# Performance work log

Hardware: AMD Instinct MI355X
Metric: run time of the kernel (lower is better)

## Reference

```python
import jax, jax.numpy as jnp
import numpy as np
import math

LMAX_IN = 3
LMAX_OUT = 2 * LMAX_IN
K_IN = (LMAX_IN + 1) ** 2      # 16
K_OUT = (LMAX_OUT + 1) ** 2    # 49
RES_BETA = 8
RES_ALPHA = 16
N = 1024
MUL = 128
C = 128
PARITY_CONFIGS = [(1, 1), (1, -1), (-1, 1)]


def _legendre(lmax, x):
    # Associated Legendre P_l^m(x) for m >= 0 (Condon-Shortley phase), numpy float64.
    P = np.zeros((lmax + 1, lmax + 1, x.shape[0]))
    s = np.sqrt(np.clip(1.0 - x * x, 0.0, 1.0))
    P[0, 0] = 1.0
    for m in range(1, lmax + 1):
        P[m, m] = -(2 * m - 1) * s * P[m - 1, m - 1]
    for m in range(lmax):
        P[m + 1, m] = (2 * m + 1) * x * P[m, m]
    for m in range(lmax + 1):
        for l in range(m + 2, lmax + 1):
            P[l, m] = ((2 * l - 1) * x * P[l - 1, m] - (l - 1 + m) * P[l - 2, m]) / (l - m)
    return P


def _real_sh(lmax, cosb, alpha):
    # Orthonormal real spherical harmonics on the (beta, alpha) grid -> [(lmax+1)^2, B*A].
    P = _legendre(lmax, cosb)
    B, A = cosb.shape[0], alpha.shape[0]
    Y = np.zeros(((lmax + 1) ** 2, B, A))
    for l in range(lmax + 1):
        for m in range(-l, l + 1):
            am = abs(m)
            norm = math.sqrt((2 * l + 1) / (4 * math.pi) * math.factorial(l - am) / math.factorial(l + am))
            if m > 0:
                az = math.sqrt(2.0) * np.cos(m * alpha)
            elif m == 0:
                az = np.ones(A)
            else:
                az = math.sqrt(2.0) * np.sin(am * alpha)
            Y[l * l + l + m] = norm * P[l, am][:, None] * az[None, :]
    return Y.reshape((lmax + 1) ** 2, B * A)


def _grids():
    # Gauss-Legendre quadrature in cos(beta), uniform azimuth -> exact band-limited transforms.
    cosb, wb = np.polynomial.legendre.leggauss(RES_BETA)
    alpha = np.linspace(0.0, 2.0 * np.pi, RES_ALPHA, endpoint=False)
    qw = (wb[:, None] * np.full((1, RES_ALPHA), 2.0 * np.pi / RES_ALPHA)).reshape(-1)
    Y_in = _real_sh(LMAX_IN, cosb, alpha)
    Y_out_w = _real_sh(LMAX_OUT, cosb, alpha) * qw[None, :]
    return Y_in.astype(np.float32), Y_out_w.astype(np.float32)


def _l_of_k(lmax):
    return np.array([l for l in range(lmax + 1) for _ in range(2 * l + 1)])


_YIN_NP, _YOW_NP = _grids()
_LK_IN = _l_of_k(LMAX_IN)
_LK_OUT = _l_of_k(LMAX_OUT)


def _project_in(x, W, p_val):
    # e3nn.flax.Linear to s2_irreps(lmax, p_val, p_arg=-1)*C : per-l pick the matching
    # parity block of the input and channel-mix it (1/sqrt(fan_in) path norm).
    pi_l = np.array([(1 - p_val * (-1) ** l) // 2 for l in range(LMAX_IN + 1)])
    pi_k = pi_l[_LK_IN]                      # [K_IN] parity slot per SH component
    x_sel = x[:, :, pi_k, np.arange(K_IN)]    # [N, MUL, K_IN]
    Wk = W[_LK_IN]                            # [K_IN, MUL, C]
    return jnp.einsum('nuk,kuc->nck', x_sel, Wk) * (1.0 / math.sqrt(MUL))


def setup_inputs() -> dict:
    key = jax.random.key(0)
    k1, k2, k3, k4, k5 = jax.random.split(key, 5)
    return {
        'input1': jax.random.normal(k1, (N, MUL, 2, K_IN), dtype=jnp.float32),
        'input2': jax.random.normal(k2, (N, MUL, 2, K_IN), dtype=jnp.float32),
        'W_in1': jax.random.normal(k3, (3, LMAX_IN + 1, MUL, C), dtype=jnp.float32),
        'W_in2': jax.random.normal(k4, (3, LMAX_IN + 1, MUL, C), dtype=jnp.float32),
        'W_out': jax.random.normal(k5, (3, LMAX_OUT + 1, C, C), dtype=jnp.float32),
    }


def reference(input1, input2, W_in1, W_in2, W_out):
    Yin = jnp.asarray(_YIN_NP)    # [K_IN, G] synthesis basis
    Yow = jnp.asarray(_YOW_NP)    # [K_OUT, G] analysis basis (quadrature-weighted)
    outs = []
    for i, (p1, p2) in enumerate(PARITY_CONFIGS):
        c1 = _project_in(input1, W_in1[i], p1)           # [N, C, K_IN]
        c2 = _project_in(input2, W_in2[i], p2)           # [N, C, K_IN]
        g1 = jnp.einsum('nck,kg->ncg', c1, Yin)          # SH synthesis on S2 grid
        g2 = jnp.einsum('nck,kg->ncg', c2, Yin)
        z = jnp.einsum('ncg,kg->nck', g1 * g2, Yow)      # pointwise mult + analysis, lmax_out = 2*lmax
        Wo = W_out[i][_LK_OUT]                            # [K_OUT, C, C]
        o = jnp.einsum('nck,kcd->ndk', z, Wo) * (1.0 / math.sqrt(C))
        outs.append(o.reshape(N, C * K_OUT))
    return jnp.concatenate(outs, axis=1)                 # [N, 3*C*K_OUT]
```

## Files before the change

### kernel.cpp

```cpp
#include <hip/hip_runtime.h>
#include <hip/hip_bf16.h>
#include <math.h>


#define PI_D 3.14159265358979323846

using short8 = __attribute__((ext_vector_type(8))) short;
using f32x4  = __attribute__((ext_vector_type(4))) float;

__device__ __host__ constexpr int lof_in(int k)  { return k>=9?3 : k>=4?2 : k>=1?1 : 0; }
__device__ __host__ constexpr int lof_out(int k) { return k>=36?6 : k>=25?5 : k>=16?4 : k>=9?3 : k>=4?2 : k>=1?1 : 0; }

__device__ __forceinline__ unsigned short f2h(float f) {
  _Float16 h = (_Float16)f;
  return __builtin_bit_cast(unsigned short, h);
}

__global__ void tables_kernel(unsigned short* __restrict__ YinH,
                              unsigned short* __restrict__ YowH)
{
  const int g = threadIdx.x;
  if (g >= 128) return;
  const int b = g >> 4;
  const int a = g & 15;

  const double xb_[8] = {
    -0.9602898564975362, -0.7966664774136267, -0.5255324099163290, -0.1834346424956498,
     0.1834346424956498,  0.5255324099163290,  0.7966664774136267,  0.9602898564975362};
  const double wb_[8] = {
     0.10122853629037626, 0.22238103445337447, 0.31370664587788729, 0.36268378337836198,
     0.36268378337836198, 0.31370664587788729, 0.22238103445337447, 0.10122853629037626};

  const double x = xb_[b];
  const double s = sqrt(fmax(0.0, 1.0 - x * x));
  const double alpha = (2.0 * PI_D / 16.0) * (double)a;

  double P[7][7];
  for (int l = 0; l < 7; ++l)
    for (int m = 0; m < 7; ++m) P[l][m] = 0.0;
  P[0][0] = 1.0;
  for (int m = 1; m <= 6; ++m) P[m][m] = -(double)(2 * m - 1) * s * P[m - 1][m - 1];
  for (int m = 0; m <= 5; ++m) P[m + 1][m] = (double)(2 * m + 1) * x * P[m][m];
  for (int m = 0; m <= 6; ++m)
    for (int l = m + 2; l <= 6; ++l)
      P[l][m] = ((double)(2 * l - 1) * x * P[l - 1][m] - (double)(l - 1 + m) * P[l - 2][m]) / (double)(l - m);

  const double qw = wb_[b] * (2.0 * PI_D / 16.0);

  for (int l = 0; l <= 6; ++l) {
    for (int m = -l; m <= l; ++m) {
      const int am = m < 0 ? -m : m;
      double fr = 1.0;
      for (int j = l - am + 1; j <= l + am; ++j) fr /= (double)j;
      const double norm = sqrt((double)(2 * l + 1) / (4.0 * PI_D) * fr);
      double az;
      if (m > 0)       az = sqrt(2.0) * cos((double)m * alpha);
      else if (m == 0) az = 1.0;
      else             az = sqrt(2.0) * sin((double)am * alpha);
      const double Y = norm * P[l][am] * az;
      const int k = l * l + l + m;
      if (l <= 3) YinH[g * 16 + k] = f2h((float)Y);
      YowH[k * 128 + g] = f2h((float)(Y * qw));
    }
  }
  for (int k = 49; k < 64; ++k) YowH[k * 128 + g] = 0;
}

__global__ void prep_wot(const float* __restrict__ Wo, unsigned short* __restrict__ WoTH)
{
  const int e = blockIdx.x * 256 + threadIdx.x;
  const int c = e & 127;
  const int d = (e >> 7) & 127;
  const int r = e >> 14;
  WoTH[((size_t)r * 128 + d) * 128 + c] = f2h(Wo[((size_t)r * 128 + c) * 128 + d]);
}

template <int IP>
__device__ __forceinline__ void stage1_body(
    int nb, int tid, float* lds,
    const float* __restrict__ x1, const float* __restrict__ x2,
    const float* __restrict__ W1, const float* __restrict__ W2,
    unsigned short* __restrict__ c1H, unsigned short* __restrict__ c2H)
{
  const int c  = tid & 127;
  const int nn = tid >> 7;
  const int n  = nb * 2 + nn;

  float c1a[16], c2a[16];
#pragma unroll
  for (int k = 0; k < 16; ++k) { c1a[k] = 0.f; c2a[k] = 0.f; }

  const float* w1b = W1 + IP * 65536 + c;
  const float* w2b = W2 + IP * 65536 + c;

  for (int uc = 0; uc < 4; ++uc) {
    __syncthreads();
#pragma unroll
    for (int i = 0; i < 8; ++i) {
      const int e   = tid + 256 * i;
      const int inp = e >> 10;
      const int r   = e & 1023;
      const int nns = r >> 9;
      const int u   = (r >> 4) & 31;
      const int k   = r & 15;
      const int l   = lof_in(k);
      const int flip = (inp == 0) ? ((IP == 2) ? 1 : 0) : ((IP == 1) ? 1 : 0);
      const int ch  = (l & 1) ^ flip;
      const float* src = (inp == 0) ? x1 : x2;
      lds[e] = src[(size_t)(nb * 2 + nns) * 4096 + uc * 1024 + u * 32 + ch * 16 + k];
    }
    __syncthreads();
    for (int uu = 0; uu < 32; ++uu) {
      const int u = uc * 32 + uu;
      float w1v[4], w2v[4];
#pragma unroll
      for (int l = 0; l < 4; ++l) {
        w1v[l] = w1b[(l * 128 + u) * 128];
        w2v[l] = w2b[(l * 128 + u) * 128];
      }
      const float4* xs1 = (const float4*)&lds[nn * 512 + uu * 16];
      const float4* xs2 = (const float4*)&lds[1024 + nn * 512 + uu * 16];
      const float4 A0 = xs1[0], A1 = xs1[1], A2 = xs1[2], A3 = xs1[3];
      const float4 B0 = xs2[0], B1 = xs2[1], B2 = xs2[2], B3 = xs2[3];
      c1a[0]  = fmaf(A0.x, w1v[0], c1a[0]);
      c1a[1]  = fmaf(A0.y, w1v[1], c1a[1]);
      c1a[2]  = fmaf(A0.z, w1v[1], c1a[2]);
      c1a[3]  = fmaf(A0.w, w1v[1], c1a[3]);
      c1a[4]  = fmaf(A1.x, w1v[2], c1a[4]);
      c1a[5]  = fmaf(A1.y, w1v[2], c1a[5]);
      c1a[6]  = fmaf(A1.z, w1v[2], c1a[6]);
      c1a[7]  = fmaf(A1.w, w1v[2], c1a[7]);
      c1a[8]  = fmaf(A2.x, w1v[2], c1a[8]);
      c1a[9]  = fmaf(A2.y, w1v[3], c1a[9]);
      c1a[10] = fmaf(A2.z, w1v[3], c1a[10]);
      c1a[11] = fmaf(A2.w, w1v[3], c1a[11]);
      c1a[12] = fmaf(A3.x, w1v[3], c1a[12]);
      c1a[13] = fmaf(A3.y, w1v[3], c1a[13]);
      c1a[14] = fmaf(A3.z, w1v[3], c1a[14]);
      c1a[15] = fmaf(A3.w, w1v[3], c1a[15]);

      c2a[0]  = fmaf(B0.x, w2v[0], c2a[0]);
      c2a[1]  = fmaf(B0.y, w2v[1], c2a[1]);
      c2a[2]  = fmaf(B0.z, w2v[1], c2a[2]);
      c2a[3]  = fmaf(B0.w, w2v[1], c2a[3]);
      c2a[4]  = fmaf(B1.x, w2v[2], c2a[4]);
      c2a[5]  = fmaf(B1.y, w2v[2], c2a[5]);
      c2a[6]  = fmaf(B1.z, w2v[2], c2a[6]);
      c2a[7]  = fmaf(B1.w, w2v[2], c2a[7]);
      c2a[8]  = fmaf(B2.x, w2v[2], c2a[8]);
      c2a[9]  = fmaf(B2.y, w2v[3], c2a[9]);
      c2a[10] = fmaf(B2.z, w2v[3], c2a[10]);
      c2a[11] = fmaf(B2.w, w2v[3], c2a[11]);
      c2a[12] = fmaf(B3.x, w2v[3], c2a[12]);
      c2a[13] = fmaf(B3.y, w2v[3], c2a[13]);
      c2a[14] = fmaf(B3.z, w2v[3], c2a[14]);
      c2a[15] = fmaf(B3.w, w2v[3], c2a[15]);
    }
  }

  const float ism = 0.08838834764831845f;
  unsigned int pk1[8], pk2[8];
#pragma unroll
  for (int q = 0; q < 8; ++q) {
    pk1[q] = (unsigned)f2h(c1a[2 * q] * ism) | ((unsigned)f2h(c1a[2 * q + 1] * ism) << 16);
    pk2[q] = (unsigned)f2h(c2a[2 * q] * ism) | ((unsigned)f2h(c2a[2 * q + 1] * ism) << 16);
  }
  const size_t ob = (((size_t)IP * 1024 + n) * 128 + c) * 16;
  uint4* o1 = (uint4*)(c1H + ob);
  uint4* o2 = (uint4*)(c2H + ob);
  o1[0] = make_uint4(pk1[0], pk1[1], pk1[2], pk1[3]);
  o1[1] = make_uint4(pk1[4], pk1[5], pk1[6], pk1[7]);
  o2[0] = make_uint4(pk2[0], pk2[1], pk2[2], pk2[3]);
  o2[1] = make_uint4(pk2[4], pk2[5], pk2[6], pk2[7]);
}

__global__ __launch_bounds__(256, 4) void stage1_kernel(
    const float* __restrict__ x1, const float* __restrict__ x2,
    const float* __restrict__ W1, const float* __restrict__ W2,
    unsigned short* __restrict__ c1H, unsigned short* __restrict__ c2H)
{
  __shared__ float lds[2048];
  const int bid = blockIdx.x;
  const int ip = bid >> 9;
  const int nb = bid & 511;
  const int tid = threadIdx.x;
  if (ip == 0)      stage1_body<0>(nb, tid, lds, x1, x2, W1, W2, c1H, c2H);
  else if (ip == 1) stage1_body<1>(nb, tid, lds, x1, x2, W1, W2, c1H, c2H);
  else              stage1_body<2>(nb, tid, lds, x1, x2, W1, W2, c1H, c2H);
}

__global__ __launch_bounds__(256, 3) void fused23_kernel(
    const unsigned short* __restrict__ c1H, const unsigned short* __restrict__ c2H,
    const unsigned short* __restrict__ YinH, const unsigned short* __restrict__ YowH,
    unsigned short* __restrict__ zH)
{
  __shared__ char Pl[32768];
  const int bid = blockIdx.x;
  const int ip  = bid >> 10;
  const int n   = bid & 1023;
  const int tid = threadIdx.x;
  const int w    = tid >> 6;
  const int lane = tid & 63;
  const int lr   = lane & 15;
  const int lg   = lane >> 4;

  const short8 Z8 = {0, 0, 0, 0, 0, 0, 0, 0};

  short8 a1[2], a2[2];
  const size_t cbase = ((size_t)ip * 1024 + n) * 128 * 16;
#pragma unroll
  for (int mti = 0; mti < 2; ++mti) {
    const int c = (2 * w + mti) * 16 + lr;
    a1[mti] = Z8; a2[mti] = Z8;
    if (lg < 2) {
      a1[mti] = *(const short8*)(c1H + cbase + (size_t)c * 16 + lg * 8);
      a2[mti] = *(const short8*)(c2H + cbase + (size_t)c * 16 + lg * 8);
    }
  }

#pragma unroll
  for (int h = 0; h < 2; ++h) {
    short8 yb[4];
#pragma unroll
    for (int gq = 0; gq < 4; ++gq) {
      const int g = (h * 4 + gq) * 16 + lr;
      yb[gq] = Z8;
      if (lg < 2) yb[gq] = *(const short8*)(YinH + (size_t)g * 16 + lg * 8);
    }
    f32x4 G1[2][4], G2[2][4];
#pragma unroll
    for (int mti = 0; mti < 2; ++mti)
#pragma unroll
      for (int gq = 0; gq < 4; ++gq) {
        G1[mti][gq] = (f32x4){0.f, 0.f, 0.f, 0.f};
        G2[mti][gq] = (f32x4){0.f, 0.f, 0.f, 0.f};
        G1[mti][gq] = __builtin_amdgcn_mfma_f32_16x16x32_f16(a1[mti], yb[gq], G1[mti][gq], 0, 0, 0);
        G2[mti][gq] = __builtin_amdgcn_mfma_f32_16x16x32_f16(a2[mti], yb[gq], G2[mti][gq], 0, 0, 0);
      }
#pragma unroll
    for (int mti = 0; mti < 2; ++mti)
#pragma unroll
      for (int gq = 0; gq < 4; ++gq) {
        const int g = (h * 4 + gq) * 16 + lr;
#pragma unroll
        for (int j = 0; j < 4; ++j) {
          const int m = (2 * w + mti) * 16 + lg * 4 + j;
          const float p = G1[mti][gq][j] * G2[mti][gq][j];
          *(unsigned short*)(Pl + m * 256 + ((g * 2) ^ ((m & 7) << 4))) = f2h(p);
        }
      }
  }
  __syncthreads();

  short8 yw[4][4];
#pragma unroll
  for (int kt = 0; kt < 4; ++kt)
#pragma unroll
    for (int ks = 0; ks < 4; ++ks)
      yw[kt][ks] = *(const short8*)(YowH + (size_t)(kt * 16 + lr) * 128 + ks * 32 + lg * 8);

  f32x4 Zc[2][4];
#pragma unroll
  for (int mti = 0; mti < 2; ++mti)
#pragma unroll
    for (int kt = 0; kt < 4; ++kt) Zc[mti][kt] = (f32x4){0.f, 0.f, 0.f, 0.f};

#pragma unroll
  for (int ks = 0; ks < 4; ++ks) {
    short8 ap[2];
#pragma unroll
    for (int mti = 0; mti < 2; ++mti) {
      const int m = (2 * w + mti) * 16 + lr;
      ap[mti] = *(const short8*)(Pl + m * 256 + ((ks * 64 + lg * 16) ^ ((m & 7) << 4)));
    }
#pragma unroll
    for (int mti = 0; mti < 2; ++mti)
#pragma unroll
      for (int kt = 0; kt < 4; ++kt)
        Zc[mti][kt] = __builtin_amdgcn_mfma_f32_16x16x32_f16(ap[mti], yw[kt][ks], Zc[mti][kt], 0, 0, 0);
  }

#pragma unroll
  for (int mti = 0; mti < 2; ++mti)
#pragma unroll
    for (int kt = 0; kt < 4; ++kt) {
      const int kout = kt * 16 + lr;
      if (kout < 49) {
        const int c0 = (2 * w + mti) * 16 + lg * 4;
        uint2 v;
        v.x = (unsigned)f2h(Zc[mti][kt][0]) | ((unsigned)f2h(Zc[mti][kt][1]) << 16);
        v.y = (unsigned)f2h(Zc[mti][kt][2]) | ((unsigned)f2h(Zc[mti][kt][3]) << 16);
        *(uint2*)(zH + (((size_t)ip * 49 + kout) * 1024 + n) * 128 + c0) = v;
      }
    }
}

__global__ __launch_bounds__(256, 3) void stage4_mfma(
    const unsigned short* __restrict__ zH, const unsigned short* __restrict__ WoTH,
    float* __restrict__ out)
{
  const int bid = blockIdx.x;
  const int ip  = bid / 392;
  const int r   = bid - ip * 392;
  const int w49 = r >> 3;
  const int nblk = r & 7;
  const int l   = lof_out(w49);
  const int tid = threadIdx.x;
  const int wv   = tid >> 6;
  const int lane = tid & 63;
  const int lr   = lane & 15;
  const int lg   = lane >> 4;

  const unsigned short* Ab = zH + (((size_t)ip * 49 + w49) * 1024 + nblk * 128) * 128;
  const unsigned short* Bb = WoTH + (size_t)(ip * 7 + l) * 128 * 128;

  f32x4 acc[2][8];
#pragma unroll
  for (int mti = 0; mti < 2; ++mti)
#pragma unroll
    for (int dt = 0; dt < 8; ++dt) acc[mti][dt] = (f32x4){0.f, 0.f, 0.f, 0.f};

#pragma unroll
  for (int ks = 0; ks < 4; ++ks) {
    short8 b[8], a[2];
#pragma unroll
    for (int dt = 0; dt < 8; ++dt)
      b[dt] = *(const short8*)(Bb + (size_t)(dt * 16 + lr) * 128 + ks * 32 + lg * 8);
#pragma unroll
    for (int mti = 0; mti < 2; ++mti)
      a[mti] = *(const short8*)(Ab + (size_t)((2 * wv + mti) * 16 + lr) * 128 + ks * 32 + lg * 8);
#pragma unroll
    for (int mti = 0; mti < 2; ++mti)
#pragma unroll
      for (int dt = 0; dt < 8; ++dt)
        acc[mti][dt] = __builtin_amdgcn_mfma_f32_16x16x32_f16(a[mti], b[dt], acc[mti][dt], 0, 0, 0);
  }

  const float isc = 0.08838834764831845f;
#pragma unroll
  for (int mti = 0; mti < 2; ++mti)
#pragma unroll
    for (int dt = 0; dt < 8; ++dt) {
      const int d = dt * 16 + lr;
#pragma unroll
      for (int j = 0; j < 4; ++j) {
        const int n = nblk * 128 + (2 * wv + mti) * 16 + lg * 4 + j;
        out[(size_t)n * 18816 + ip * 6272 + d * 49 + w49] = acc[mti][dt][j] * isc;
      }
    }
}

extern "C" void kernel_launch(void* const* d_in, const int* in_sizes, int n_in,
                              void* d_out, int out_size, void* d_ws, size_t ws_size,
                              hipStream_t stream)
{
  const float* x1 = (const float*)d_in[0];
  const float* x2 = (const float*)d_in[1];
  const float* W1 = (const float*)d_in[2];
  const float* W2 = (const float*)d_in[3];
  const float* Wo = (const float*)d_in[4];
  float* out = (float*)d_out;

  char* ws = (char*)d_ws;
  unsigned short* YinH = (unsigned short*)(ws);
  unsigned short* YowH = (unsigned short*)(ws + 16384);
  unsigned short* WoTH = (unsigned short*)(ws + 49152);
  unsigned short* c1H  = (unsigned short*)(ws + (1u << 20));
  unsigned short* c2H  = (unsigned short*)(ws + (1u << 24));
  unsigned short* zH   = (unsigned short*)(ws + (1u << 25));

  tables_kernel<<<1, 128, 0, stream>>>(YinH, YowH);
  prep_wot<<<1344, 256, 0, stream>>>(Wo, WoTH);
  stage1_kernel<<<1536, 256, 0, stream>>>(x1, x2, W1, W2, c1H, c2H);
  fused23_kernel<<<3072, 256, 0, stream>>>(c1H, c2H, YinH, YowH, zH);
  stage4_mfma<<<1176, 256, 0, stream>>>(zH, WoTH, out);
}
```

Baseline: 416.4 us.

## Move input projection to MFMA, parallelize SH tables, restructure output GEMM tiling

Replaces the scalar FMA input projection with fp16 MFMA GEMMs. This needs new kernels that pre-transpose the weights and the inputs into fp16 layouts grouped by k. The table kernel now spreads each (grid point, k) pair across threads instead of one thread looping serially. The output projection kernel is retiled so each block loops over all 49 k values for one d-tile, reusing B fragments per l. Risks: inputs are now quantized to fp16, the new k-major scatter stores to c1H and out are strided, and the extra launches add overhead.

```diff
diff --git a/kernel.cpp b/kernel.cpp
--- a/kernel.cpp
+++ b/kernel.cpp
@@ -16,11 +16,13 @@
   return __builtin_bit_cast(unsigned short, h);
 }
 
-__global__ void tables_kernel(unsigned short* __restrict__ YinH,
-                              unsigned short* __restrict__ YowH)
-{
-  const int g = threadIdx.x;
-  if (g >= 128) return;
+__global__ void tables2(unsigned short* __restrict__ YinH,
+                        unsigned short* __restrict__ YowH)
+{
+  const int g = blockIdx.x;
+  const int t = threadIdx.x;
+  if (t >= 64 || g >= 128) return;
+
   const int b = g >> 4;
   const int a = g & 15;
 
@@ -31,39 +33,40 @@
      0.10122853629037626, 0.22238103445337447, 0.31370664587788729, 0.36268378337836198,
      0.36268378337836198, 0.31370664587788729, 0.22238103445337447, 0.10122853629037626};
 
+  if (t >= 49) {
+    YowH[t * 128 + g] = 0;
+    return;
+  }
+
+  const int l  = lof_out(t);
+  const int m  = t - l * l - l;
+  const int am = m < 0 ? -m : m;
+
   const double x = xb_[b];
   const double s = sqrt(fmax(0.0, 1.0 - x * x));
   const double alpha = (2.0 * PI_D / 16.0) * (double)a;
 
-  double P[7][7];
-  for (int l = 0; l < 7; ++l)
-    for (int m = 0; m < 7; ++m) P[l][m] = 0.0;
-  P[0][0] = 1.0;
-  for (int m = 1; m <= 6; ++m) P[m][m] = -(double)(2 * m - 1) * s * P[m - 1][m - 1];
-  for (int m = 0; m <= 5; ++m) P[m + 1][m] = (double)(2 * m + 1) * x * P[m][m];
-  for (int m = 0; m <= 6; ++m)
-    for (int l = m + 2; l <= 6; ++l)
-      P[l][m] = ((double)(2 * l - 1) * x * P[l - 1][m] - (double)(l - 1 + m) * P[l - 2][m]) / (double)(l - m);
-
+  double pmm = 1.0;
+  for (int j = 1; j <= am; ++j) pmm = -(double)(2 * j - 1) * s * pmm;
+  double p = pmm, pm1 = 0.0;
+  for (int ll = am; ll < l; ++ll) {
+    double pn = ((double)(2 * ll + 1) * x * p - (double)(ll + am) * pm1) / (double)(ll + 1 - am);
+    pm1 = p; p = pn;
+  }
+
+  double fr = 1.0;
+  for (int j = l - am + 1; j <= l + am; ++j) fr /= (double)j;
+  const double norm = sqrt((double)(2 * l + 1) / (4.0 * PI_D) * fr);
+  double az;
+  if (m > 0)       az = sqrt(2.0) * cos((double)m * alpha);
+  else if (m == 0) az = 1.0;
+  else             az = sqrt(2.0) * sin((double)am * alpha);
+
+  const double Y  = norm * p * az;
   const double qw = wb_[b] * (2.0 * PI_D / 16.0);
 
-  for (int l = 0; l <= 6; ++l) {
-    for (int m = -l; m <= l; ++m) {
-      const int am = m < 0 ? -m : m;
-      double fr = 1.0;
-      for (int j = l - am + 1; j <= l + am; ++j) fr /= (double)j;
-      const double norm = sqrt((double)(2 * l + 1) / (4.0 * PI_D) * fr);
-      double az;
-      if (m > 0)       az = sqrt(2.0) * cos((double)m * alpha);
-      else if (m == 0) az = 1.0;
-      else             az = sqrt(2.0) * sin((double)am * alpha);
-      const double Y = norm * P[l][am] * az;
-      const int k = l * l + l + m;
-      if (l <= 3) YinH[g * 16 + k] = f2h((float)Y);
-      YowH[k * 128 + g] = f2h((float)(Y * qw));
-    }
-  }
-  for (int k = 49; k < 64; ++k) YowH[k * 128 + g] = 0;
+  if (t < 16) YinH[g * 16 + t] = f2h((float)Y);
+  YowH[t * 128 + g] = f2h((float)(Y * qw));
 }
 
 __global__ void prep_wot(const float* __restrict__ Wo, unsigned short* __restrict__ WoTH)
@@ -75,118 +78,111 @@
   WoTH[((size_t)r * 128 + d) * 128 + c] = f2h(Wo[((size_t)r * 128 + c) * 128 + d]);
 }
 
-template <int IP>
-__device__ __forceinline__ void stage1_body(
-    int nb, int tid, float* lds,
+__global__ void prep_win(const float* __restrict__ W1, const float* __restrict__ W2,
+                         unsigned short* __restrict__ WtIn)
+{
+  const int e = blockIdx.x * 256 + threadIdx.x;
+  const int u = e & 127;
+  const int c = (e >> 7) & 127;
+  const int r = e >> 14;
+  const int in = r / 12;
+  const int rr = r - in * 12;
+  const float* W = (in == 0) ? W1 : W2;
+  WtIn[e] = f2h(W[((size_t)rr * 128 + u) * 128 + c]);
+}
+
+__global__ __launch_bounds__(256) void transpose_x(
     const float* __restrict__ x1, const float* __restrict__ x2,
-    const float* __restrict__ W1, const float* __restrict__ W2,
-    unsigned short* __restrict__ c1H, unsigned short* __restrict__ c2H)
-{
-  const int c  = tid & 127;
-  const int nn = tid >> 7;
-  const int n  = nb * 2 + nn;
-
-  float c1a[16], c2a[16];
-#pragma unroll
-  for (int k = 0; k < 16; ++k) { c1a[k] = 0.f; c2a[k] = 0.f; }
-
-  const float* w1b = W1 + IP * 65536 + c;
-  const float* w2b = W2 + IP * 65536 + c;
-
-  for (int uc = 0; uc < 4; ++uc) {
-    __syncthreads();
-#pragma unroll
-    for (int i = 0; i < 8; ++i) {
-      const int e   = tid + 256 * i;
-      const int inp = e >> 10;
-      const int r   = e & 1023;
-      const int nns = r >> 9;
-      const int u   = (r >> 4) & 31;
-      const int k   = r & 15;
-      const int l   = lof_in(k);
-      const int flip = (inp == 0) ? ((IP == 2) ? 1 : 0) : ((IP == 1) ? 1 : 0);
-      const int ch  = (l & 1) ^ flip;
-      const float* src = (inp == 0) ? x1 : x2;
-      lds[e] = src[(size_t)(nb * 2 + nns) * 4096 + uc * 1024 + u * 32 + ch * 16 + k];
-    }
-    __syncthreads();
-    for (int uu = 0; uu < 32; ++uu) {
-      const int u = uc * 32 + uu;
-      float w1v[4], w2v[4];
-#pragma unroll
-      for (int l = 0; l < 4; ++l) {
-        w1v[l] = w1b[(l * 128 + u) * 128];
-        w2v[l] = w2b[(l * 128 + u) * 128];
-      }
-      const float4* xs1 = (const float4*)&lds[nn * 512 + uu * 16];
-      const float4* xs2 = (const float4*)&lds[1024 + nn * 512 + uu * 16];
-      const float4 A0 = xs1[0], A1 = xs1[1], A2 = xs1[2], A3 = xs1[3];
-      const float4 B0 = xs2[0], B1 = xs2[1], B2 = xs2[2], B3 = xs2[3];
-      c1a[0]  = fmaf(A0.x, w1v[0], c1a[0]);
-      c1a[1]  = fmaf(A0.y, w1v[1], c1a[1]);
-      c1a[2]  = fmaf(A0.z, w1v[1], c1a[2]);
-      c1a[3]  = fmaf(A0.w, w1v[1], c1a[3]);
-      c1a[4]  = fmaf(A1.x, w1v[2], c1a[4]);
-      c1a[5]  = fmaf(A1.y, w1v[2], c1a[5]);
-      c1a[6]  = fmaf(A1.z, w1v[2], c1a[6]);
-      c1a[7]  = fmaf(A1.w, w1v[2], c1a[7]);
-      c1a[8]  = fmaf(A2.x, w1v[2], c1a[8]);
-      c1a[9]  = fmaf(A2.y, w1v[3], c1a[9]);
-      c1a[10] = fmaf(A2.z, w1v[3], c1a[10]);
-      c1a[11] = fmaf(A2.w, w1v[3], c1a[11]);
-      c1a[12] = fmaf(A3.x, w1v[3], c1a[12]);
-      c1a[13] = fmaf(A3.y, w1v[3], c1a[13]);
-      c1a[14] = fmaf(A3.z, w1v[3], c1a[14]);
-      c1a[15] = fmaf(A3.w, w1v[3], c1a[15]);
-
-      c2a[0]  = fmaf(B0.x, w2v[0], c2a[0]);
-      c2a[1]  = fmaf(B0.y, w2v[1], c2a[1]);
-      c2a[2]  = fmaf(B0.z, w2v[1], c2a[2]);
-      c2a[3]  = fmaf(B0.w, w2v[1], c2a[3]);
-      c2a[4]  = fmaf(B1.x, w2v[2], c2a[4]);
-      c2a[5]  = fmaf(B1.y, w2v[2], c2a[5]);
-      c2a[6]  = fmaf(B1.z, w2v[2], c2a[6]);
-      c2a[7]  = fmaf(B1.w, w2v[2], c2a[7]);
-      c2a[8]  = fmaf(B2.x, w2v[2], c2a[8]);
-      c2a[9]  = fmaf(B2.y, w2v[3], c2a[9]);
-      c2a[10] = fmaf(B2.z, w2v[3], c2a[10]);
-      c2a[11] = fmaf(B2.w, w2v[3], c2a[11]);
-      c2a[12] = fmaf(B3.x, w2v[3], c2a[12]);
-      c2a[13] = fmaf(B3.y, w2v[3], c2a[13]);
-      c2a[14] = fmaf(B3.z, w2v[3], c2a[14]);
-      c2a[15] = fmaf(B3.w, w2v[3], c2a[15]);
-    }
-  }
-
-  const float ism = 0.08838834764831845f;
-  unsigned int pk1[8], pk2[8];
-#pragma unroll
-  for (int q = 0; q < 8; ++q) {
-    pk1[q] = (unsigned)f2h(c1a[2 * q] * ism) | ((unsigned)f2h(c1a[2 * q + 1] * ism) << 16);
-    pk2[q] = (unsigned)f2h(c2a[2 * q] * ism) | ((unsigned)f2h(c2a[2 * q + 1] * ism) << 16);
-  }
-  const size_t ob = (((size_t)IP * 1024 + n) * 128 + c) * 16;
-  uint4* o1 = (uint4*)(c1H + ob);
-  uint4* o2 = (uint4*)(c2H + ob);
-  o1[0] = make_uint4(pk1[0], pk1[1], pk1[2], pk1[3]);
-  o1[1] = make_uint4(pk1[4], pk1[5], pk1[6], pk1[7]);
-  o2[0] = make_uint4(pk2[0], pk2[1], pk2[2], pk2[3]);
-  o2[1] = make_uint4(pk2[4], pk2[5], pk2[6], pk2[7]);
-}
-
-__global__ __launch_bounds__(256, 4) void stage1_kernel(
-    const float* __restrict__ x1, const float* __restrict__ x2,
-    const float* __restrict__ W1, const float* __restrict__ W2,
-    unsigned short* __restrict__ c1H, unsigned short* __restrict__ c2H)
-{
-  __shared__ float lds[2048];
+    unsigned short* __restrict__ xT)
+{
   const int bid = blockIdx.x;
-  const int ip = bid >> 9;
+  const int in = bid >> 9;
   const int nb = bid & 511;
   const int tid = threadIdx.x;
-  if (ip == 0)      stage1_body<0>(nb, tid, lds, x1, x2, W1, W2, c1H, c2H);
-  else if (ip == 1) stage1_body<1>(nb, tid, lds, x1, x2, W1, W2, c1H, c2H);
-  else              stage1_body<2>(nb, tid, lds, x1, x2, W1, W2, c1H, c2H);
+  const int ug  = tid >> 5;
+  const int chk = tid & 31;
+  const float* src = ((in == 0) ? x1 : x2) + (size_t)nb * 2 * 4096;
+  unsigned short* dst = xT + (size_t)in * 2 * 16 * 1024 * 128;
+
+#pragma unroll
+  for (int n = 0; n < 2; ++n) {
+    unsigned int w[8];
+#pragma unroll
+    for (int q = 0; q < 8; ++q) {
+      const int u0 = ug * 16 + 2 * q;
+      const unsigned short lo = f2h(src[n * 4096 + (u0 + 0) * 32 + chk]);
+      const unsigned short hi = f2h(src[n * 4096 + (u0 + 1) * 32 + chk]);
+      w[q] = (unsigned)lo | ((unsigned)hi << 16);
+    }
+    unsigned short* pd = dst + (((size_t)chk * 1024 + nb * 2 + n) * 128 + ug * 16);
+    ((uint4*)pd)[0] = make_uint4(w[0], w[1], w[2], w[3]);
+    ((uint4*)pd)[1] = make_uint4(w[4], w[5], w[6], w[7]);
+  }
+}
+
+__global__ __launch_bounds__(256) void stage1_mfma(
+    const unsigned short* __restrict__ xT, const unsigned short* __restrict__ WtIn,
+    unsigned short* __restrict__ c1H, unsigned short* __restrict__ c2H)
+{
+  const int bid = blockIdx.x;
+  const int l  = bid & 3;
+  const int nt = (bid >> 2) & 15;
+  const int in = (bid >> 6) & 1;
+  const int ip = bid >> 7;
+  const int tid  = threadIdx.x;
+  const int wv   = tid >> 6;
+  const int lane = tid & 63;
+  const int lr   = lane & 15;
+  const int lg   = lane >> 4;
+  const int n0   = nt * 64 + wv * 16;
+
+  const int flip = (in == 0) ? (ip == 2 ? 1 : 0) : (ip == 1 ? 1 : 0);
+  const int ch   = (l & 1) ^ flip;
+
+  const unsigned short* A0 = xT + ((size_t)in * 2 + ch) * 16 * 1024 * 128;
+  const unsigned short* B0 = WtIn + (((size_t)in * 3 + ip) * 4 + l) * 128 * 128;
+  unsigned short* outp = ((in == 0) ? c1H : c2H) + (size_t)ip * 1024 * 128 * 16;
+
+  const int kcnt  = 2 * l + 1;
+  const int kbase = l * l;
+  const float ism = 0.08838834764831845f;
+
+#pragma unroll
+  for (int cp = 0; cp < 2; ++cp) {
+    short8 bf[4][4];
+#pragma unroll
+    for (int ct = 0; ct < 4; ++ct)
+#pragma unroll
+      for (int ks = 0; ks < 4; ++ks)
+        bf[ct][ks] = *(const short8*)(B0 + (size_t)(cp * 64 + ct * 16 + lr) * 128 + ks * 32 + lg * 8);
+
+    for (int kk = 0; kk < kcnt; ++kk) {
+      const int k = kbase + kk;
+      short8 af[4];
+#pragma unroll
+      for (int ks = 0; ks < 4; ++ks)
+        af[ks] = *(const short8*)(A0 + ((size_t)k * 1024 + n0 + lr) * 128 + ks * 32 + lg * 8);
+
+      f32x4 acc[4];
+#pragma unroll
+      for (int ct = 0; ct < 4; ++ct) acc[ct] = (f32x4){0.f, 0.f, 0.f, 0.f};
+#pragma unroll
+      for (int ks = 0; ks < 4; ++ks)
+#pragma unroll
+        for (int ct = 0; ct < 4; ++ct)
+          acc[ct] = __builtin_amdgcn_mfma_f32_16x16x32_f16(af[ks], bf[ct][ks], acc[ct], 0, 0, 0);
+
+#pragma unroll
+      for (int ct = 0; ct < 4; ++ct) {
+        const int c = cp * 64 + ct * 16 + lr;
+#pragma unroll
+        for (int j = 0; j < 4; ++j) {
+          const int n = n0 + lg * 4 + j;
+          outp[((size_t)n * 128 + c) * 16 + k] = f2h(acc[ct][j] * ism);
+        }
+      }
+    }
+  }
 }
 
 __global__ __launch_bounds__(256, 3) void fused23_kernel(
@@ -295,59 +291,52 @@
     }
 }
 
-__global__ __launch_bounds__(256, 3) void stage4_mfma(
+__global__ __launch_bounds__(256) void stage4_v2(
     const unsigned short* __restrict__ zH, const unsigned short* __restrict__ WoTH,
     float* __restrict__ out)
 {
   const int bid = blockIdx.x;
-  const int ip  = bid / 392;
-  const int r   = bid - ip * 392;
-  const int w49 = r >> 3;
-  const int nblk = r & 7;
-  const int l   = lof_out(w49);
-  const int tid = threadIdx.x;
+  const int dt = bid & 7;
+  const int nt = (bid >> 3) & 15;
+  const int ip = bid >> 7;
+  const int tid  = threadIdx.x;
   const int wv   = tid >> 6;
   const int lane = tid & 63;
   const int lr   = lane & 15;
   const int lg   = lane >> 4;
-
-  const unsigned short* Ab = zH + (((size_t)ip * 49 + w49) * 1024 + nblk * 128) * 128;
-  const unsigned short* Bb = WoTH + (size_t)(ip * 7 + l) * 128 * 128;
-
-  f32x4 acc[2][8];
-#pragma unroll
-  for (int mti = 0; mti < 2; ++mti)
-#pragma unroll
-    for (int dt = 0; dt < 8; ++dt) acc[mti][dt] = (f32x4){0.f, 0.f, 0.f, 0.f};
-
-#pragma unroll
-  for (int ks = 0; ks < 4; ++ks) {
-    short8 b[8], a[2];
-#pragma unroll
-    for (int dt = 0; dt < 8; ++dt)
-      b[dt] = *(const short8*)(Bb + (size_t)(dt * 16 + lr) * 128 + ks * 32 + lg * 8);
-#pragma unroll
-    for (int mti = 0; mti < 2; ++mti)
-      a[mti] = *(const short8*)(Ab + (size_t)((2 * wv + mti) * 16 + lr) * 128 + ks * 32 + lg * 8);
-#pragma unroll
-    for (int mti = 0; mti < 2; ++mti)
-#pragma unroll
-      for (int dt = 0; dt < 8; ++dt)
-        acc[mti][dt] = __builtin_amdgcn_mfma_f32_16x16x32_f16(a[mti], b[dt], acc[mti][dt], 0, 0, 0);
-  }
-
+  const int n0   = nt * 64 + wv * 16;
+  const int d    = dt * 16 + lr;
+
+  const unsigned short* Bb = WoTH + (size_t)ip * 7 * 16384;
   const float isc = 0.08838834764831845f;
-#pragma unroll
-  for (int mti = 0; mti < 2; ++mti)
-#pragma unroll
-    for (int dt = 0; dt < 8; ++dt) {
-      const int d = dt * 16 + lr;
+
+  for (int l = 0; l <= 6; ++l) {
+    short8 bf[4];
+#pragma unroll
+    for (int ks = 0; ks < 4; ++ks)
+      bf[ks] = *(const short8*)(Bb + (size_t)l * 16384 + (size_t)(dt * 16 + lr) * 128 + ks * 32 + lg * 8);
+
+    const int kcnt = 2 * l + 1;
+    for (int kk = 0; kk < kcnt; ++kk) {
+      const int k = l * l + kk;
+      const unsigned short* Ab = zH + ((size_t)ip * 49 + k) * 1024 * 128;
+      short8 af[4];
+#pragma unroll
+      for (int ks = 0; ks < 4; ++ks)
+        af[ks] = *(const short8*)(Ab + (size_t)(n0 + lr) * 128 + ks * 32 + lg * 8);
+
+      f32x4 acc = (f32x4){0.f, 0.f, 0.f, 0.f};
+#pragma unroll
+      for (int ks = 0; ks < 4; ++ks)
+        acc = __builtin_amdgcn_mfma_f32_16x16x32_f16(af[ks], bf[ks], acc, 0, 0, 0);
+
 #pragma unroll
       for (int j = 0; j < 4; ++j) {
-        const int n = nblk * 128 + (2 * wv + mti) * 16 + lg * 4 + j;
-        out[(size_t)n * 18816 + ip * 6272 + d * 49 + w49] = acc[mti][dt][j] * isc;
-      }
-    }
+        const int n = n0 + lg * 4 + j;
+        out[(size_t)n * 18816 + ip * 6272 + d * 49 + k] = acc[j] * isc;
+      }
+    }
+  }
 }
 
 extern "C" void kernel_launch(void* const* d_in, const int* in_sizes, int n_in,
@@ -364,14 +353,18 @@
   char* ws = (char*)d_ws;
   unsigned short* YinH = (unsigned short*)(ws);
   unsigned short* YowH = (unsigned short*)(ws + 16384);
-  unsigned short* WoTH = (unsigned short*)(ws + 49152);
-  unsigned short* c1H  = (unsigned short*)(ws + (1u << 20));
-  unsigned short* c2H  = (unsigned short*)(ws + (1u << 24));
-  unsigned short* zH   = (unsigned short*)(ws + (1u << 25));
-
-  tables_kernel<<<1, 128, 0, stream>>>(YinH, YowH);
+  unsigned short* WoTH = (unsigned short*)(ws + 65536);
+  unsigned short* WtIn = (unsigned short*)(ws + 786432);
+  unsigned short* xT   = (unsigned short*)(ws + 2097152);
+  unsigned short* c1H  = (unsigned short*)(ws + 18874368);
+  unsigned short* c2H  = (unsigned short*)(ws + 31457280);
+  unsigned short* zH   = (unsigned short*)(ws + 44040192);
+
+  tables2<<<128, 64, 0, stream>>>(YinH, YowH);
   prep_wot<<<1344, 256, 0, stream>>>(Wo, WoTH);
-  stage1_kernel<<<1536, 256, 0, stream>>>(x1, x2, W1, W2, c1H, c2H);
+  prep_win<<<1536, 256, 0, stream>>>(W1, W2, WtIn);
+  transpose_x<<<1024, 256, 0, stream>>>(x1, x2, xT);
+  stage1_mfma<<<384, 256, 0, stream>>>(xT, WtIn, c1H, c2H);
   fused23_kernel<<<3072, 256, 0, stream>>>(c1H, c2H, YinH, YowH, zH);
-  stage4_mfma<<<1176, 256, 0, stream>>>(zH, WoTH, out);
-}
+  stage4_v2<<<384, 256, 0, stream>>>(zH, WoTH, out);
+}
```

After: 576.1 us. +38.4%, slower.
